# Kernel optimization log

Measured on AMD Instinct MI355X. Metric: run time of the kernel, lower is better.

Reference implementation:

```python
import jax, jax.numpy as jnp
import numpy as np

N_NODES = 100000
N_EDGES = 1250000
IN_CH = 64
OUT_CH = 64


def setup_inputs() -> dict:
    key = jax.random.key(0)
    k1, k2, k3 = jax.random.split(key, 3)
    x = jax.random.normal(k1, (N_NODES, IN_CH), dtype=jnp.float32)
    edge_index = jax.random.randint(k2, (2, N_EDGES), 0, N_NODES, dtype=jnp.int64)
    # torch.nn.Linear(3*IN_CH, OUT_CH): W [out, in], b [out]
    scale = 1.0 / np.sqrt(3 * IN_CH)
    W = jax.random.uniform(k3, (OUT_CH, 3 * IN_CH), dtype=jnp.float32,
                           minval=-scale, maxval=scale)
    b = jnp.zeros((OUT_CH,), dtype=jnp.float32)
    return {"x": x, "edge_index": edge_index, "W": W, "b": b}


def reference(x, edge_index, W, b):
    src, dst = edge_index[0], edge_index[1]
    msgs = x[src]  # [E, D] gather of source node features

    agg_sum = jax.ops.segment_sum(msgs, dst, num_segments=N_NODES)  # [N, D]
    count = jax.ops.segment_sum(jnp.ones((msgs.shape[0],), dtype=x.dtype),
                                dst, num_segments=N_NODES)  # [N]
    agg_mean = agg_sum / jnp.maximum(count, 1.0)[:, None]

    agg_max = jax.ops.segment_max(msgs, dst, num_segments=N_NODES)  # [N, D]
    has_edge = (count > 0)[:, None]
    agg_max = jnp.where(has_edge, agg_max, 0.0)  # empty segments -> 0 (PyG default)

    feats = jnp.concatenate([agg_sum, agg_mean, agg_max], axis=-1)  # [N, 3D]
    return jnp.einsum('nf,of->no', feats, W) + b
```

## Files before the change

kernel.cpp:

```cpp
#include <hip/hip_runtime.h>
#include <hip/hip_bf16.h>
#include <math.h>

#define D    64
#define F3   192
#define NPB  256
#define LBITS 8
#define SBITS 17
#define NBLK 256
#define SCAN_CHUNK 2048

using bf16x8 = __attribute__((ext_vector_type(8))) short;
using f32x4  = __attribute__((ext_vector_type(4))) float;


__global__ __launch_bounds__(256) void k_bin_hist(
    const int* __restrict__ dstv, unsigned* __restrict__ bcntT,
    int E, int EPB, int NB)
{
    __shared__ unsigned h[512];
    for (int i = threadIdx.x; i < NB; i += 256) h[i] = 0;
    __syncthreads();
    int lo = blockIdx.x * EPB, hi = min(E, lo + EPB);
    for (int e = lo + threadIdx.x; e < hi; e += 256)
        atomicAdd(&h[((unsigned)dstv[e]) >> LBITS], 1u);
    __syncthreads();
    for (int i = threadIdx.x; i < NB; i += 256)
        bcntT[(size_t)i * NBLK + blockIdx.x] = h[i];
}

__global__ __launch_bounds__(256) void k_chunk_scan(
    const unsigned* __restrict__ cnt, unsigned* __restrict__ offs,
    unsigned* __restrict__ partials, int N)
{
    __shared__ unsigned ts[256];
    int t = threadIdx.x;
    int ebase = blockIdx.x * SCAN_CHUNK + t * 8;
    unsigned v[8];
    unsigned s = 0;
    #pragma unroll
    for (int j = 0; j < 8; ++j) {
        unsigned c = (ebase + j < N) ? cnt[ebase + j] : 0u;
        v[j] = s; s += c;
    }
    ts[t] = s;
    __syncthreads();
    #pragma unroll
    for (int off = 1; off < 256; off <<= 1) {
        unsigned add = (t >= off) ? ts[t - off] : 0u;
        __syncthreads();
        ts[t] += add;
        __syncthreads();
    }
    unsigned tb = (t > 0) ? ts[t - 1] : 0u;
    #pragma unroll
    for (int j = 0; j < 8; ++j)
        if (ebase + j < N) offs[ebase + j] = tb + v[j];
    if (t == 255) partials[blockIdx.x] = ts[255];
}

__global__ void k_scan_partials(unsigned* partials, int n)
{
    if (blockIdx.x == 0 && threadIdx.x == 0) {
        unsigned s = 0;
        for (int i = 0; i < n; ++i) { unsigned c = partials[i]; partials[i] = s; s += c; }
    }
}

__global__ __launch_bounds__(256) void k_add_base(
    unsigned* __restrict__ offs, const unsigned* __restrict__ partials, int N)
{
    int i = blockIdx.x * 256 + threadIdx.x;
    if (i < N) offs[i] += partials[i / SCAN_CHUNK];
}

__global__ __launch_bounds__(256) void k_bin_scatter(
    const int* __restrict__ srcv, const int* __restrict__ dstv,
    const unsigned* __restrict__ bbaseT, unsigned* __restrict__ binned,
    int E, int EPB, int NB)
{
    __shared__ unsigned cur[512];
    for (int i = threadIdx.x; i < NB; i += 256)
        cur[i] = bbaseT[(size_t)i * NBLK + blockIdx.x];
    __syncthreads();
    int lo = blockIdx.x * EPB, hi = min(E, lo + EPB);
    for (int e = lo + threadIdx.x; e < hi; e += 256) {
        unsigned d = (unsigned)dstv[e];
        unsigned s = (unsigned)srcv[e];
        unsigned p = atomicAdd(&cur[d >> LBITS], 1u);
        binned[p] = ((d & (NPB - 1u)) << SBITS) | s;
    }
}

__global__ __launch_bounds__(256) void k_bucket_csr(
    const unsigned* __restrict__ binned, const unsigned* __restrict__ bbaseT,
    unsigned* __restrict__ offs, unsigned* __restrict__ cnt,
    unsigned* __restrict__ ssrc, int E, int NB, int N)
{
    __shared__ unsigned c[256];
    __shared__ unsigned ts[256];
    int k = blockIdx.x;
    int t = threadIdx.x;
    unsigned bstart = bbaseT[(size_t)k * NBLK];
    unsigned bend   = (k + 1 < NB) ? bbaseT[(size_t)(k + 1) * NBLK] : (unsigned)E;

    c[t] = 0;
    __syncthreads();
    for (unsigned e = bstart + t; e < bend; e += 256)
        atomicAdd(&c[binned[e] >> SBITS], 1u);
    __syncthreads();

    unsigned myc = c[t];
    ts[t] = myc;
    __syncthreads();
    #pragma unroll
    for (int off = 1; off < 256; off <<= 1) {
        unsigned add = (t >= off) ? ts[t - off] : 0u;
        __syncthreads();
        ts[t] += add;
        __syncthreads();
    }
    unsigned excl = t ? ts[t - 1] : 0u;

    int gn = k * NPB + t;
    if (gn < N) { offs[gn] = bstart + excl; cnt[gn] = myc; }

    c[t] = excl;
    __syncthreads();
    for (unsigned e = bstart + t; e < bend; e += 256) {
        unsigned u  = binned[e];
        unsigned ld = u >> SBITS;
        unsigned r  = atomicAdd(&c[ld], 1u);
        ssrc[bstart + r] = u & ((1u << SBITS) - 1u);
    }
}


__device__ __forceinline__ ushort f2bf(float f) {
    __hip_bfloat16 h = __float2bfloat16(f);
    return *reinterpret_cast<ushort*>(&h);
}

__global__ __launch_bounds__(256) void k_gather(
    const float*    __restrict__ x,
    const unsigned* __restrict__ ssrc,
    const unsigned* __restrict__ offs,
    const unsigned* __restrict__ cnt,
    ushort*         __restrict__ feats,
    int N)
{
    int tid  = threadIdx.x;
    int lane = tid & 63;
    int wv   = tid >> 6;
    int g    = lane >> 4;
    int c4   = (lane & 15) << 2;

    int n = blockIdx.x * 4 + wv;
    if (n >= N) return;

    unsigned st = offs[n];
    unsigned dg = cnt[n];

    float4 sv = make_float4(0.f, 0.f, 0.f, 0.f);
    float4 mv = make_float4(-INFINITY, -INFINITY, -INFINITY, -INFINITY);

    for (unsigned i = (unsigned)g; i < dg; i += 4) {
        unsigned s = ssrc[st + i];
        float4 v = *reinterpret_cast<const float4*>(x + (size_t)s * D + c4);
        sv.x += v.x; sv.y += v.y; sv.z += v.z; sv.w += v.w;
        mv.x = fmaxf(mv.x, v.x); mv.y = fmaxf(mv.y, v.y);
        mv.z = fmaxf(mv.z, v.z); mv.w = fmaxf(mv.w, v.w);
    }

    #pragma unroll
    for (int off = 16; off <= 32; off <<= 1) {
        sv.x += __shfl_xor(sv.x, off); sv.y += __shfl_xor(sv.y, off);
        sv.z += __shfl_xor(sv.z, off); sv.w += __shfl_xor(sv.w, off);
        mv.x = fmaxf(mv.x, __shfl_xor(mv.x, off));
        mv.y = fmaxf(mv.y, __shfl_xor(mv.y, off));
        mv.z = fmaxf(mv.z, __shfl_xor(mv.z, off));
        mv.w = fmaxf(mv.w, __shfl_xor(mv.w, off));
    }

    float inv = dg ? 1.0f / (float)dg : 0.0f;
    size_t rb = (size_t)n * F3;
    if (g == 0) {
        ushort4 u = { f2bf(sv.x), f2bf(sv.y), f2bf(sv.z), f2bf(sv.w) };
        *reinterpret_cast<ushort4*>(feats + rb + c4) = u;
    } else if (g == 1) {
        ushort4 u = { f2bf(sv.x * inv), f2bf(sv.y * inv),
                      f2bf(sv.z * inv), f2bf(sv.w * inv) };
        *reinterpret_cast<ushort4*>(feats + rb + D + c4) = u;
    } else if (g == 2) {
        float4 m = mv;
        if (dg == 0) m = make_float4(0.f, 0.f, 0.f, 0.f);
        ushort4 u = { f2bf(m.x), f2bf(m.y), f2bf(m.z), f2bf(m.w) };
        *reinterpret_cast<ushort4*>(feats + rb + 2 * D + c4) = u;
    }
}

__global__ __launch_bounds__(256) void k_mlp_mfma(
    const ushort* __restrict__ feats,
    const float*  __restrict__ W,
    const float*  __restrict__ bias,
    float*        __restrict__ out,
    int N)
{
    int tid  = threadIdx.x;
    int lane = tid & 63;
    int c    = tid >> 6;
    int l16  = lane & 15;
    int kb   = (lane >> 4) << 3;

    int col = (c << 4) + l16;
    const float* wrow = W + (size_t)col * F3;

    bf16x8 bfr[6];
    #pragma unroll
    for (int ks = 0; ks < 6; ++ks) {
        float4 lo = *reinterpret_cast<const float4*>(wrow + ks * 32 + kb);
        float4 hi = *reinterpret_cast<const float4*>(wrow + ks * 32 + kb + 4);
        bf16x8 bb;
        bb[0] = (short)f2bf(lo.x); bb[1] = (short)f2bf(lo.y);
        bb[2] = (short)f2bf(lo.z); bb[3] = (short)f2bf(lo.w);
        bb[4] = (short)f2bf(hi.x); bb[5] = (short)f2bf(hi.y);
        bb[6] = (short)f2bf(hi.z); bb[7] = (short)f2bf(hi.w);
        bfr[ks] = bb;
    }
    float bo = bias[col];

    int ntiles = N >> 4;
    for (int t = blockIdx.x; t < ntiles; t += gridDim.x) {
        int n0 = t << 4;
        const ushort* arow = feats + (size_t)(n0 + l16) * F3 + kb;
        bf16x8 afr[6];
        #pragma unroll
        for (int ks = 0; ks < 6; ++ks)
            afr[ks] = *reinterpret_cast<const bf16x8*>(arow + ks * 32);

        f32x4 acc = { bo, bo, bo, bo };
        #pragma unroll
        for (int ks = 0; ks < 6; ++ks)
            acc = __builtin_amdgcn_mfma_f32_16x16x32_bf16(afr[ks], bfr[ks], acc, 0, 0, 0);

        int rbase = n0 + ((lane >> 4) << 2);
        #pragma unroll
        for (int r = 0; r < 4; ++r)
            out[(size_t)(rbase + r) * D + col] = acc[r];
    }
}

extern "C" void kernel_launch(void* const* d_in, const int* in_sizes, int n_in,
                              void* d_out, int out_size, void* d_ws, size_t ws_size,
                              hipStream_t stream)
{
    const float* x  = (const float*)d_in[0];
    const int*   ei = (const int*)d_in[1];
    const float* W  = (const float*)d_in[2];
    const float* b  = (const float*)d_in[3];
    float* out = (float*)d_out;

    int N = in_sizes[0] / D;
    int E = in_sizes[1] / 2;
    const int* srcv = ei;
    const int* dstv = ei + E;

    int NB  = (N + NPB - 1) / NPB;
    int EPB = (E + NBLK - 1) / NBLK;
    int M   = NB * NBLK;

    unsigned* bcntT    = (unsigned*)d_ws;
    unsigned* bbaseT   = bcntT + M;
    unsigned* partials = bbaseT + M;
    unsigned* offs     = partials + 64;
    unsigned* cnt      = offs + N;
    unsigned* ssrc     = cnt + N;
    unsigned* binned   = ssrc + E;
    ushort*   feats    = (ushort*)(binned + E);

    int nChunksM = (M + SCAN_CHUNK - 1) / SCAN_CHUNK;

    k_bin_hist<<<NBLK, 256, 0, stream>>>(dstv, bcntT, E, EPB, NB);
    k_chunk_scan<<<nChunksM, 256, 0, stream>>>(bcntT, bbaseT, partials, M);
    k_scan_partials<<<1, 64, 0, stream>>>(partials, nChunksM);
    k_add_base<<<(M + 255) / 256, 256, 0, stream>>>(bbaseT, partials, M);
    k_bin_scatter<<<NBLK, 256, 0, stream>>>(srcv, dstv, bbaseT, binned, E, EPB, NB);
    k_bucket_csr<<<NB, 256, 0, stream>>>(binned, bbaseT, offs, cnt, ssrc, E, NB, N);

    k_gather<<<(N + 3) / 4, 256, 0, stream>>>(x, ssrc, offs, cnt, feats, N);
    k_mlp_mfma<<<1024, 256, 0, stream>>>(feats, W, b, out, N);
}
```

Baseline: 133.4 us.

## Gather from bf16 copy of x, store only sum/max, fold scan-base add

Adds a pre-pass that casts x and W to bf16, so the gather reads half the bytes per neighbour row. Each lane now handles 8 channels and loads two neighbours per iteration. The stored feature row shrinks to sum and max, and the mean is rebuilt in the MLP from sum and degree. The separate add-base scan kernel is removed by adding partials inline, and the MLP runs one tile per block with preconverted bf16 weights. The cast pass costs an extra full read and write of x, and bf16 inputs together with a recomputed mean add rounding error.

```diff
diff --git a/kernel.cpp b/kernel.cpp
--- a/kernel.cpp
+++ b/kernel.cpp
@@ -4,6 +4,7 @@
 
 #define D    64
 #define F3   192
+#define FS   128
 #define NPB  256
 #define LBITS 8
 #define SBITS 17
@@ -11,7 +12,33 @@
 #define SCAN_CHUNK 2048
 
 using bf16x8 = __attribute__((ext_vector_type(8))) short;
+using u16x8  = __attribute__((ext_vector_type(8))) unsigned short;
 using f32x4  = __attribute__((ext_vector_type(4))) float;
+
+__device__ __forceinline__ ushort f2bf(float f) {
+    __hip_bfloat16 h = __float2bfloat16(f);
+    return *reinterpret_cast<ushort*>(&h);
+}
+__device__ __forceinline__ float bf2f(ushort u) {
+    unsigned v = ((unsigned)u) << 16;
+    return __uint_as_float(v);
+}
+
+__global__ __launch_bounds__(256) void k_cast(
+    const float* __restrict__ x, ushort* __restrict__ xb, int n4,
+    const float* __restrict__ W, ushort* __restrict__ Wb, int nW)
+{
+    if ((int)blockIdx.x < (n4 + 255) / 256) {
+        int i = blockIdx.x * 256 + threadIdx.x;
+        if (i < n4) {
+            float4 v = *reinterpret_cast<const float4*>(x + (size_t)i * 4);
+            ushort4 u = { f2bf(v.x), f2bf(v.y), f2bf(v.z), f2bf(v.w) };
+            *reinterpret_cast<ushort4*>(xb + (size_t)i * 4) = u;
+        }
+    } else {
+        for (int i = threadIdx.x; i < nW; i += 256) Wb[i] = f2bf(W[i]);
+    }
+}
 
 
 __global__ __launch_bounds__(256) void k_bin_hist(
@@ -67,21 +94,16 @@
     }
 }
 
-__global__ __launch_bounds__(256) void k_add_base(
-    unsigned* __restrict__ offs, const unsigned* __restrict__ partials, int N)
-{
-    int i = blockIdx.x * 256 + threadIdx.x;
-    if (i < N) offs[i] += partials[i / SCAN_CHUNK];
-}
-
 __global__ __launch_bounds__(256) void k_bin_scatter(
     const int* __restrict__ srcv, const int* __restrict__ dstv,
-    const unsigned* __restrict__ bbaseT, unsigned* __restrict__ binned,
-    int E, int EPB, int NB)
+    const unsigned* __restrict__ bbaseT, const unsigned* __restrict__ partials,
+    unsigned* __restrict__ binned, int E, int EPB, int NB)
 {
     __shared__ unsigned cur[512];
-    for (int i = threadIdx.x; i < NB; i += 256)
-        cur[i] = bbaseT[(size_t)i * NBLK + blockIdx.x];
+    for (int i = threadIdx.x; i < NB; i += 256) {
+        unsigned idx = (unsigned)i * NBLK + blockIdx.x;
+        cur[i] = bbaseT[idx] + partials[idx >> 11];
+    }
     __syncthreads();
     int lo = blockIdx.x * EPB, hi = min(E, lo + EPB);
     for (int e = lo + threadIdx.x; e < hi; e += 256) {
@@ -94,6 +116,7 @@
 
 __global__ __launch_bounds__(256) void k_bucket_csr(
     const unsigned* __restrict__ binned, const unsigned* __restrict__ bbaseT,
+    const unsigned* __restrict__ partials,
     unsigned* __restrict__ offs, unsigned* __restrict__ cnt,
     unsigned* __restrict__ ssrc, int E, int NB, int N)
 {
@@ -101,8 +124,13 @@
     __shared__ unsigned ts[256];
     int k = blockIdx.x;
     int t = threadIdx.x;
-    unsigned bstart = bbaseT[(size_t)k * NBLK];
-    unsigned bend   = (k + 1 < NB) ? bbaseT[(size_t)(k + 1) * NBLK] : (unsigned)E;
+    unsigned i0 = (unsigned)k * NBLK;
+    unsigned bstart = bbaseT[i0] + partials[i0 >> 11];
+    unsigned bend;
+    if (k + 1 < NB) {
+        unsigned i1 = (unsigned)(k + 1) * NBLK;
+        bend = bbaseT[i1] + partials[i1 >> 11];
+    } else bend = (unsigned)E;
 
     c[t] = 0;
     __syncthreads();
@@ -135,14 +163,8 @@
     }
 }
 
-
-__device__ __forceinline__ ushort f2bf(float f) {
-    __hip_bfloat16 h = __float2bfloat16(f);
-    return *reinterpret_cast<ushort*>(&h);
-}
-
-__global__ __launch_bounds__(256) void k_gather(
-    const float*    __restrict__ x,
+__global__ __launch_bounds__(256) void k_gather2(
+    const ushort*   __restrict__ xb,
     const unsigned* __restrict__ ssrc,
     const unsigned* __restrict__ offs,
     const unsigned* __restrict__ cnt,
@@ -152,8 +174,8 @@
     int tid  = threadIdx.x;
     int lane = tid & 63;
     int wv   = tid >> 6;
-    int g    = lane >> 4;
-    int c4   = (lane & 15) << 2;
+    int grp  = lane >> 3;
+    int ch8  = (lane & 7) << 3;
 
     int n = blockIdx.x * 4 + wv;
     if (n >= N) return;
@@ -161,93 +183,110 @@
     unsigned st = offs[n];
     unsigned dg = cnt[n];
 
-    float4 sv = make_float4(0.f, 0.f, 0.f, 0.f);
-    float4 mv = make_float4(-INFINITY, -INFINITY, -INFINITY, -INFINITY);
-
-    for (unsigned i = (unsigned)g; i < dg; i += 4) {
-        unsigned s = ssrc[st + i];
-        float4 v = *reinterpret_cast<const float4*>(x + (size_t)s * D + c4);
-        sv.x += v.x; sv.y += v.y; sv.z += v.z; sv.w += v.w;
-        mv.x = fmaxf(mv.x, v.x); mv.y = fmaxf(mv.y, v.y);
-        mv.z = fmaxf(mv.z, v.z); mv.w = fmaxf(mv.w, v.w);
-    }
-
-    #pragma unroll
-    for (int off = 16; off <= 32; off <<= 1) {
-        sv.x += __shfl_xor(sv.x, off); sv.y += __shfl_xor(sv.y, off);
-        sv.z += __shfl_xor(sv.z, off); sv.w += __shfl_xor(sv.w, off);
-        mv.x = fmaxf(mv.x, __shfl_xor(mv.x, off));
-        mv.y = fmaxf(mv.y, __shfl_xor(mv.y, off));
-        mv.z = fmaxf(mv.z, __shfl_xor(mv.z, off));
-        mv.w = fmaxf(mv.w, __shfl_xor(mv.w, off));
-    }
-
-    float inv = dg ? 1.0f / (float)dg : 0.0f;
-    size_t rb = (size_t)n * F3;
-    if (g == 0) {
-        ushort4 u = { f2bf(sv.x), f2bf(sv.y), f2bf(sv.z), f2bf(sv.w) };
-        *reinterpret_cast<ushort4*>(feats + rb + c4) = u;
-    } else if (g == 1) {
-        ushort4 u = { f2bf(sv.x * inv), f2bf(sv.y * inv),
-                      f2bf(sv.z * inv), f2bf(sv.w * inv) };
-        *reinterpret_cast<ushort4*>(feats + rb + D + c4) = u;
-    } else if (g == 2) {
-        float4 m = mv;
-        if (dg == 0) m = make_float4(0.f, 0.f, 0.f, 0.f);
-        ushort4 u = { f2bf(m.x), f2bf(m.y), f2bf(m.z), f2bf(m.w) };
-        *reinterpret_cast<ushort4*>(feats + rb + 2 * D + c4) = u;
-    }
-}
-
-__global__ __launch_bounds__(256) void k_mlp_mfma(
-    const ushort* __restrict__ feats,
-    const float*  __restrict__ W,
-    const float*  __restrict__ bias,
-    float*        __restrict__ out,
+    float s[8], m[8];
+    #pragma unroll
+    for (int j = 0; j < 8; ++j) { s[j] = 0.0f; m[j] = -INFINITY; }
+
+    unsigned i = (unsigned)grp;
+    for (; i + 8 < dg; i += 16) {
+        unsigned s0 = ssrc[st + i];
+        unsigned s1 = ssrc[st + i + 8];
+        u16x8 a = *reinterpret_cast<const u16x8*>(xb + (size_t)s0 * D + ch8);
+        u16x8 b = *reinterpret_cast<const u16x8*>(xb + (size_t)s1 * D + ch8);
+        #pragma unroll
+        for (int j = 0; j < 8; ++j) {
+            float fa = bf2f(a[j]), fb = bf2f(b[j]);
+            s[j] += fa + fb;
+            m[j] = fmaxf(m[j], fmaxf(fa, fb));
+        }
+    }
+    if (i < dg) {
+        unsigned s0 = ssrc[st + i];
+        u16x8 a = *reinterpret_cast<const u16x8*>(xb + (size_t)s0 * D + ch8);
+        #pragma unroll
+        for (int j = 0; j < 8; ++j) {
+            float fa = bf2f(a[j]);
+            s[j] += fa;
+            m[j] = fmaxf(m[j], fa);
+        }
+    }
+
+    #pragma unroll
+    for (int off = 8; off <= 32; off <<= 1) {
+        #pragma unroll
+        for (int j = 0; j < 8; ++j) {
+            s[j] += __shfl_xor(s[j], off);
+            m[j] = fmaxf(m[j], __shfl_xor(m[j], off));
+        }
+    }
+
+    if (grp == 0) {
+        u16x8 u;
+        #pragma unroll
+        for (int j = 0; j < 8; ++j) u[j] = f2bf(s[j]);
+        *reinterpret_cast<u16x8*>(feats + (size_t)n * FS + ch8) = u;
+    } else if (grp == 1) {
+        u16x8 u;
+        #pragma unroll
+        for (int j = 0; j < 8; ++j) u[j] = dg ? f2bf(m[j]) : (ushort)0;
+        *reinterpret_cast<u16x8*>(feats + (size_t)n * FS + 64 + ch8) = u;
+    }
+}
+
+__global__ __launch_bounds__(256) void k_mlp2(
+    const ushort*   __restrict__ feats,
+    const unsigned* __restrict__ cnt,
+    const ushort*   __restrict__ Wb,
+    const float*    __restrict__ bias,
+    float*          __restrict__ out,
     int N)
 {
     int tid  = threadIdx.x;
     int lane = tid & 63;
-    int c    = tid >> 6;
+    int wv   = tid >> 6;
     int l16  = lane & 15;
     int kb   = (lane >> 4) << 3;
 
-    int col = (c << 4) + l16;
-    const float* wrow = W + (size_t)col * F3;
-
-    bf16x8 bfr[6];
-    #pragma unroll
-    for (int ks = 0; ks < 6; ++ks) {
-        float4 lo = *reinterpret_cast<const float4*>(wrow + ks * 32 + kb);
-        float4 hi = *reinterpret_cast<const float4*>(wrow + ks * 32 + kb + 4);
-        bf16x8 bb;
-        bb[0] = (short)f2bf(lo.x); bb[1] = (short)f2bf(lo.y);
-        bb[2] = (short)f2bf(lo.z); bb[3] = (short)f2bf(lo.w);
-        bb[4] = (short)f2bf(hi.x); bb[5] = (short)f2bf(hi.y);
-        bb[6] = (short)f2bf(hi.z); bb[7] = (short)f2bf(hi.w);
-        bfr[ks] = bb;
-    }
+    int col = (wv << 4) + l16;
+    const ushort* wp = Wb + (size_t)col * F3 + kb;
+    bf16x8 bS0 = *reinterpret_cast<const bf16x8*>(wp);
+    bf16x8 bS1 = *reinterpret_cast<const bf16x8*>(wp + 32);
+    bf16x8 bM0 = *reinterpret_cast<const bf16x8*>(wp + 64);
+    bf16x8 bM1 = *reinterpret_cast<const bf16x8*>(wp + 96);
+    bf16x8 bX0 = *reinterpret_cast<const bf16x8*>(wp + 128);
+    bf16x8 bX1 = *reinterpret_cast<const bf16x8*>(wp + 160);
     float bo = bias[col];
 
-    int ntiles = N >> 4;
-    for (int t = blockIdx.x; t < ntiles; t += gridDim.x) {
-        int n0 = t << 4;
-        const ushort* arow = feats + (size_t)(n0 + l16) * F3 + kb;
-        bf16x8 afr[6];
-        #pragma unroll
-        for (int ks = 0; ks < 6; ++ks)
-            afr[ks] = *reinterpret_cast<const bf16x8*>(arow + ks * 32);
-
-        f32x4 acc = { bo, bo, bo, bo };
-        #pragma unroll
-        for (int ks = 0; ks < 6; ++ks)
-            acc = __builtin_amdgcn_mfma_f32_16x16x32_bf16(afr[ks], bfr[ks], acc, 0, 0, 0);
-
-        int rbase = n0 + ((lane >> 4) << 2);
-        #pragma unroll
-        for (int r = 0; r < 4; ++r)
-            out[(size_t)(rbase + r) * D + col] = acc[r];
-    }
+    int n0 = blockIdx.x << 4;
+
+    unsigned dgr = cnt[n0 + l16];
+    float inv = dgr ? 1.0f / (float)dgr : 0.0f;
+
+    const ushort* arow = feats + (size_t)(n0 + l16) * FS + kb;
+    bf16x8 aS0 = *reinterpret_cast<const bf16x8*>(arow);
+    bf16x8 aS1 = *reinterpret_cast<const bf16x8*>(arow + 32);
+    bf16x8 aX0 = *reinterpret_cast<const bf16x8*>(arow + 64);
+    bf16x8 aX1 = *reinterpret_cast<const bf16x8*>(arow + 96);
+
+    bf16x8 aM0, aM1;
+    #pragma unroll
+    for (int j = 0; j < 8; ++j) {
+        aM0[j] = (short)f2bf(bf2f((ushort)aS0[j]) * inv);
+        aM1[j] = (short)f2bf(bf2f((ushort)aS1[j]) * inv);
+    }
+
+    f32x4 acc = { bo, bo, bo, bo };
+    acc = __builtin_amdgcn_mfma_f32_16x16x32_bf16(aS0, bS0, acc, 0, 0, 0);
+    acc = __builtin_amdgcn_mfma_f32_16x16x32_bf16(aS1, bS1, acc, 0, 0, 0);
+    acc = __builtin_amdgcn_mfma_f32_16x16x32_bf16(aM0, bM0, acc, 0, 0, 0);
+    acc = __builtin_amdgcn_mfma_f32_16x16x32_bf16(aM1, bM1, acc, 0, 0, 0);
+    acc = __builtin_amdgcn_mfma_f32_16x16x32_bf16(aX0, bX0, acc, 0, 0, 0);
+    acc = __builtin_amdgcn_mfma_f32_16x16x32_bf16(aX1, bX1, acc, 0, 0, 0);
+
+    int rbase = n0 + ((lane >> 4) << 2);
+    #pragma unroll
+    for (int r = 0; r < 4; ++r)
+        out[(size_t)(rbase + r) * D + col] = acc[r];
 }
 
 extern "C" void kernel_launch(void* const* d_in, const int* in_sizes, int n_in,
@@ -276,17 +315,21 @@
     unsigned* cnt      = offs + N;
     unsigned* ssrc     = cnt + N;
     unsigned* binned   = ssrc + E;
-    ushort*   feats    = (ushort*)(binned + E);
+    ushort*   xb       = (ushort*)(binned + E);
+    ushort*   Wb       = xb + (size_t)N * D;
+    ushort*   feats    = Wb + (size_t)D * F3;
 
     int nChunksM = (M + SCAN_CHUNK - 1) / SCAN_CHUNK;
+    int n4 = N * D / 4;
+
+    k_cast<<<(n4 + 255) / 256 + 1, 256, 0, stream>>>(x, xb, n4, W, Wb, D * F3);
 
     k_bin_hist<<<NBLK, 256, 0, stream>>>(dstv, bcntT, E, EPB, NB);
     k_chunk_scan<<<nChunksM, 256, 0, stream>>>(bcntT, bbaseT, partials, M);
     k_scan_partials<<<1, 64, 0, stream>>>(partials, nChunksM);
-    k_add_base<<<(M + 255) / 256, 256, 0, stream>>>(bbaseT, partials, M);
-    k_bin_scatter<<<NBLK, 256, 0, stream>>>(srcv, dstv, bbaseT, binned, E, EPB, NB);
-    k_bucket_csr<<<NB, 256, 0, stream>>>(binned, bbaseT, offs, cnt, ssrc, E, NB, N);
-
-    k_gather<<<(N + 3) / 4, 256, 0, stream>>>(x, ssrc, offs, cnt, feats, N);
-    k_mlp_mfma<<<1024, 256, 0, stream>>>(feats, W, b, out, N);
-}
+    k_bin_scatter<<<NBLK, 256, 0, stream>>>(srcv, dstv, bbaseT, partials, binned, E, EPB, NB);
+    k_bucket_csr<<<NB, 256, 0, stream>>>(binned, bbaseT, partials, offs, cnt, ssrc, E, NB, N);
+
+    k_gather2<<<(N + 3) / 4, 256, 0, stream>>>(xb, ssrc, offs, cnt, feats, N);
+    k_mlp2<<<N / 16, 256, 0, stream>>>(feats, cnt, Wb, b, out, N);
+}
```

Result: slower. 142.8 us (+7.0%).
